# Kernel tuning notes

Measured on AMD Instinct MI355X. Metric: run time of the kernel, lower is better.

## Reference

```python
import jax, jax.numpy as jnp
import numpy as np

S = 4            # scale_factor (conv-transpose stride)
K = 5            # kernel_size
PAD = 1 + (K - S - 1) // 2   # = 1
OP = (K - S) % 2             # = 1 (output_padding)
SCALE_SPACE = 0.1
SCALE_COLOR = 0.5


def setup_inputs() -> dict:
    key = jax.random.key(0)
    k1, k2 = jax.random.split(key)
    x = jax.random.normal(k1, (4, 1, 128, 128), dtype=jnp.float32)
    hr_guidance = jax.random.uniform(k2, (4, 3, 512, 512), dtype=jnp.float32)
    # convt.weight after __init__ fill: identity across channels, all-ones over KxK window
    weight = jnp.ones((1, 1, K, K), dtype=jnp.float32)
    return {"x": x, "hr_guidance": hr_guidance, "weight": weight}


def _valid_1d(n):
    # Indicator over the padded, stride-inserted axis (length n+K-1): positions that
    # hold real low-res samples (mask_pattern of packernel2d, transposed nd2col of ones).
    pad_lo = (K - 1) - PAD
    n_lo = (n + 2 * PAD - OP - (K - 1) - 1) // S + 1   # back-computed low-res size
    n_up = (n_lo - 1) * S + 1                          # stride-inserted size
    idx = jnp.arange(n + K - 1) - pad_lo
    return ((idx >= 0) & (idx < n_up) & (idx % S == 0)).astype(jnp.float32)


def _bilateral_kernel(G):
    # G: (bs, C, H, W) scaled guidance features -> normalized PAC kernel (bs, K*K, H, W)
    bs, C, H, W = G.shape
    r = (K - 1) // 2                                   # guidance unfold padding (k-1)*d//2
    Gp = jnp.pad(G, ((0, 0), (0, 0), (r, r), (r, r)))
    # gaussian of guidance differences; the center-tap feature equals G itself
    kern = jnp.stack([jnp.exp(-0.5 * jnp.sum((Gp[:, :, i:i + H, j:j + W] - G) ** 2, axis=1))
                      for i in range(K) for j in range(K)], axis=1)   # (bs, K*K, H, W)
    mh, mw = _valid_1d(H), _valid_1d(W)
    mask = jnp.stack([mh[i:i + H][:, None] * mw[j:j + W][None, :]
                      for i in range(K) for j in range(K)], axis=0)   # (K*K, H, W)
    kern = kern * mask[None]
    norm = jnp.sum(kern, axis=1, keepdims=True)        # normalize_kernel=True
    return kern / (norm + (norm == 0).astype(kern.dtype))


def _upsample_pad(x, H, W):
    # zero-insertion by stride S plus the padding conv_transpose implies
    bs, ch, h, w = x.shape
    pad_lo = (K - 1) - PAD
    Xp = jnp.zeros((bs, ch, H + K - 1, W + K - 1), x.dtype)
    return Xp.at[:, :, pad_lo:pad_lo + S * (h - 1) + 1:S,
                 pad_lo:pad_lo + S * (w - 1) + 1:S].set(x)


def reference(x, hr_guidance, weight):
    bs, cg, H, W = hr_guidance.shape
    hh = jnp.arange(H, dtype=hr_guidance.dtype)
    ww = jnp.arange(W, dtype=hr_guidance.dtype)
    G = jnp.concatenate([
        hr_guidance * SCALE_COLOR,
        jnp.broadcast_to(hh[None, None, :, None] * SCALE_SPACE, (bs, 1, H, W)),
        jnp.broadcast_to(ww[None, None, None, :] * SCALE_SPACE, (bs, 1, H, W)),
    ], axis=1)                                         # (bs, cg+2, H, W)
    kern = _bilateral_kernel(G)                        # (bs, K*K, H, W)
    Xp = _upsample_pad(x, H, W)
    cols = jnp.stack([Xp[:, 0, i:i + H, j:j + W]
                      for i in range(K) for j in range(K)], axis=1)   # (bs, K*K, H, W)
    # conv_transpose weight -> correlation weight: swap in/out channels, flip taps
    w_flat = weight.transpose(1, 0, 2, 3)[:, :, ::-1, ::-1].reshape(-1)  # (K*K,)
    out = jnp.einsum('bkhw,k->bhw', kern * cols, w_flat)
    return out[:, None]                                # (bs, 1, H, W)
```

## Files before the change

### kernel.cpp

```cpp
#include <hip/hip_runtime.h>


#define HW_ (512 * 512)
#define XLW 128

__global__ __launch_bounds__(256) void jbu_kernel(
    const float* __restrict__ x,
    const float* __restrict__ guide,
    const float* __restrict__ weight,
    float* __restrict__ out)
{
    int idx = blockIdx.x * blockDim.x + threadIdx.x;
    int w = idx & 511;
    int h = (idx >> 9) & 511;
    int b = idx >> 18;

    const float* gb = guide + (size_t)b * 3 * HW_;
    int cidx = h * 512 + w;
    float g0 = gb[cidx];
    float g1 = gb[HW_ + cidx];
    float g2 = gb[2 * HW_ + cidx];

    int i0 = (3 - (h & 3)) & 3;
    int ni = 1 + (int)(i0 == 0 && h < 508);
    int j0 = (3 - (w & 3)) & 3;
    int nj = 1 + (int)(j0 == 0 && w < 508);

    const float* xb = x + b * (XLW * XLW);

    float acc = 0.0f, norm = 0.0f;
    #pragma unroll
    for (int ti = 0; ti < 2; ++ti) {
        if (ti >= ni) break;
        int i  = i0 + 4 * ti;
        int a  = (h + i - 3) >> 2;
        int hn = h + i - 2;
        float di = (float)(i - 2);
        float di2 = 0.01f * di * di;
        #pragma unroll
        for (int tj = 0; tj < 2; ++tj) {
            if (tj >= nj) break;
            int j  = j0 + 4 * tj;
            int c  = (w + j - 3) >> 2;
            int wn = w + j - 2;
            float dj = (float)(j - 2);
            int nidx = hn * 512 + wn;
            float d0 = gb[nidx]           - g0;
            float d1 = gb[HW_ + nidx]     - g1;
            float d2c = gb[2 * HW_ + nidx] - g2;
            float dist = 0.25f * (d0 * d0 + d1 * d1 + d2c * d2c)
                       + di2 + 0.01f * dj * dj;
            float kv = __expf(-0.5f * dist);
            norm += kv;
            acc  += kv * xb[a * XLW + c] * weight[(4 - i) * 5 + (4 - j)];
        }
    }
    out[idx] = acc / norm;
}

extern "C" void kernel_launch(void* const* d_in, const int* in_sizes, int n_in,
                              void* d_out, int out_size, void* d_ws, size_t ws_size,
                              hipStream_t stream) {
    const float* x      = (const float*)d_in[0];
    const float* guide  = (const float*)d_in[1];
    const float* weight = (const float*)d_in[2];
    float* out = (float*)d_out;

    int total = 4 * 512 * 512;
    (void)in_sizes; (void)n_in; (void)out_size; (void)d_ws; (void)ws_size;
    jbu_kernel<<<total / 256, 256, 0, stream>>>(x, guide, weight, out);
}
```

Baseline: 72.02 us.

## Compute four adjacent output pixels per thread with float4 guidance loads

Each thread now handles four horizontally adjacent output pixels in one 4-wide phase group. Those pixels share the same low-res neighbor samples, so the neighbor guidance values and x samples are loaded once and reused across them. Center guidance is read and output written with float4 vector accesses. The grid shrinks fourfold, and the change relies on hand-derived tap indexing and spatial constants, which risks subtle correctness errors at phase and boundary edges.

```diff
diff --git a/kernel.cpp b/kernel.cpp
--- a/kernel.cpp
+++ b/kernel.cpp
@@ -2,7 +2,6 @@
 
 
 #define HW_ (512 * 512)
-#define XLW 128
 
 __global__ __launch_bounds__(256) void jbu_kernel(
     const float* __restrict__ x,
@@ -10,52 +9,80 @@
     const float* __restrict__ weight,
     float* __restrict__ out)
 {
-    int idx = blockIdx.x * blockDim.x + threadIdx.x;
-    int w = idx & 511;
-    int h = (idx >> 9) & 511;
-    int b = idx >> 18;
+    int tid = blockIdx.x * blockDim.x + threadIdx.x;
+    int m = tid & 127;
+    int h = (tid >> 7) & 511;
+    int b = tid >> 16;
+    int q = h >> 2, rh = h & 3;
 
     const float* gb = guide + (size_t)b * 3 * HW_;
-    int cidx = h * 512 + w;
-    float g0 = gb[cidx];
-    float g1 = gb[HW_ + cidx];
-    float g2 = gb[2 * HW_ + cidx];
+    const float* xb = x + b * 128 * 128;
 
-    int i0 = (3 - (h & 3)) & 3;
-    int ni = 1 + (int)(i0 == 0 && h < 508);
-    int j0 = (3 - (w & 3)) & 3;
-    int nj = 1 + (int)(j0 == 0 && w < 508);
+    int cbase = h * 512 + 4 * m;
+    float4 c0 = *(const float4*)(gb + cbase);
+    float4 c1 = *(const float4*)(gb + HW_ + cbase);
+    float4 c2 = *(const float4*)(gb + 2 * HW_ + cbase);
+    float cc0[4] = {c0.x, c0.y, c0.z, c0.w};
+    float cc1[4] = {c1.x, c1.y, c1.z, c1.w};
+    float cc2[4] = {c2.x, c2.y, c2.z, c2.w};
 
-    const float* xb = x + b * (XLW * XLW);
+    bool cs = (m < 127);
+    int  co = cs ? 4 : 0;
+    int  xo = cs ? 1 : 0;
+    float csf = cs ? 1.0f : 0.0f;
 
-    float acc = 0.0f, norm = 0.0f;
+    int sr = (4 * q + 1) * 512 + 4 * m + 1;
+    float s00_0 = gb[sr],      s00_1 = gb[HW_ + sr],      s00_2 = gb[2 * HW_ + sr];
+    float s01_0 = gb[sr + co], s01_1 = gb[HW_ + sr + co], s01_2 = gb[2 * HW_ + sr + co];
+    float x00 = xb[q * 128 + m];
+    float x01 = xb[q * 128 + m + xo];
+
+    int dip = ((3 - rh) & 3) - 2;
+    float spr0 = 0.005f * (float)(dip * dip);
+    const float spcl[4] = {0.005f, 0.0f, 0.005f, 0.02f};
+
+    int i0wi = rh + 1;
+    float wr0[5], wr1[5];
     #pragma unroll
-    for (int ti = 0; ti < 2; ++ti) {
-        if (ti >= ni) break;
-        int i  = i0 + 4 * ti;
-        int a  = (h + i - 3) >> 2;
-        int hn = h + i - 2;
-        float di = (float)(i - 2);
-        float di2 = 0.01f * di * di;
+    for (int k = 0; k < 5; ++k) { wr0[k] = weight[i0wi * 5 + k]; wr1[k] = weight[k]; }
+
+    float acc[4] = {0, 0, 0, 0}, nrm[4] = {0, 0, 0, 0};
+
+    #pragma unroll
+    for (int p = 0; p < 4; ++p) {
+        float d0 = s00_0 - cc0[p], d1 = s00_1 - cc1[p], d2 = s00_2 - cc2[p];
+        float kv = __expf(-0.125f * (d0*d0 + d1*d1 + d2*d2) - spr0 - spcl[p]) * wr0[p + 1];
+        nrm[p] += kv; acc[p] += kv * x00;
+    }
+    {
+        float d0 = s01_0 - cc0[3], d1 = s01_1 - cc1[3], d2 = s01_2 - cc2[3];
+        float kv = __expf(-0.125f * (d0*d0 + d1*d1 + d2*d2) - spr0 - 0.02f) * wr0[0] * csf;
+        nrm[3] += kv; acc[3] += kv * x01;
+    }
+
+    if (rh == 3 && q < 127) {
+        int sr1 = sr + 4 * 512;
+        float s10_0 = gb[sr1],      s10_1 = gb[HW_ + sr1],      s10_2 = gb[2 * HW_ + sr1];
+        float s11_0 = gb[sr1 + co], s11_1 = gb[HW_ + sr1 + co], s11_2 = gb[2 * HW_ + sr1 + co];
+        float x10 = xb[(q + 1) * 128 + m];
+        float x11 = xb[(q + 1) * 128 + m + xo];
         #pragma unroll
-        for (int tj = 0; tj < 2; ++tj) {
-            if (tj >= nj) break;
-            int j  = j0 + 4 * tj;
-            int c  = (w + j - 3) >> 2;
-            int wn = w + j - 2;
-            float dj = (float)(j - 2);
-            int nidx = hn * 512 + wn;
-            float d0 = gb[nidx]           - g0;
-            float d1 = gb[HW_ + nidx]     - g1;
-            float d2c = gb[2 * HW_ + nidx] - g2;
-            float dist = 0.25f * (d0 * d0 + d1 * d1 + d2c * d2c)
-                       + di2 + 0.01f * dj * dj;
-            float kv = __expf(-0.5f * dist);
-            norm += kv;
-            acc  += kv * xb[a * XLW + c] * weight[(4 - i) * 5 + (4 - j)];
+        for (int p = 0; p < 4; ++p) {
+            float d0 = s10_0 - cc0[p], d1 = s10_1 - cc1[p], d2 = s10_2 - cc2[p];
+            float kv = __expf(-0.125f * (d0*d0 + d1*d1 + d2*d2) - 0.02f - spcl[p]) * wr1[p + 1];
+            nrm[p] += kv; acc[p] += kv * x10;
         }
+        float d0 = s11_0 - cc0[3], d1 = s11_1 - cc1[3], d2 = s11_2 - cc2[3];
+        float kv = __expf(-0.125f * (d0*d0 + d1*d1 + d2*d2) - 0.04f) * wr1[0] * csf;
+        nrm[3] += kv; acc[3] += kv * x11;
     }
-    out[idx] = acc / norm;
+
+    float4 o;
+    o.x = acc[0] / nrm[0];
+    o.y = acc[1] / nrm[1];
+    o.z = acc[2] / nrm[2];
+    o.w = acc[3] / nrm[3];
+    *(float4*)(out + (size_t)b * HW_ + cbase) = o;
 }
 
 extern "C" void kernel_launch(void* const* d_in, const int* in_sizes, int n_in,
@@ -66,7 +93,7 @@
     const float* weight = (const float*)d_in[2];
     float* out = (float*)d_out;
 
-    int total = 4 * 512 * 512;
     (void)in_sizes; (void)n_in; (void)out_size; (void)d_ws; (void)ws_size;
+    int total = 4 * 512 * 128;
     jbu_kernel<<<total / 256, 256, 0, stream>>>(x, guide, weight, out);
 }
```

New measurement: 69.43 us. -3.6%, faster.
